# Kernel tuning notes

Hardware: AMD Instinct MI355X
Metric: run time of the kernel (lower is better)

Reference implementation:

```python
import jax, jax.numpy as jnp
import numpy as np

N_RET = 8192
N_LGN = 2048
SQUARE_SIZE = 10.0
NEIGHBOURHOOD = 1.0
MU_WTS = 2.5
SIGMA_WTS = 0.14
ETA = 0.1


def setup_inputs() -> dict:
    key = jax.random.key(0)
    ks = jax.random.split(key, 6)
    # retina topology on a [0, square_size]^2 plane
    topo = jax.random.uniform(ks[0], (N_RET, 2), dtype=jnp.float32) * SQUARE_SIZE
    # pairwise distances [N_ret, N_ret]
    d = jnp.sqrt(jnp.sum((topo[:, None, :] - topo[None, :, :]) ** 2, axis=-1))
    # per-node neighbourhood weights: normal(mu, sigma) masked to dist <= neighbourhood_size
    w = MU_WTS + SIGMA_WTS * jax.random.normal(ks[1], (N_RET, N_RET), dtype=jnp.float32)
    retina_weights = jnp.where(d <= NEIGHBOURHOOD, w, 0.0)
    # per-node firing threshold (Node internals: threshold ~ N(70, 2), same family as LGN)
    retina_threshold = 70.0 + 2.0 * jax.random.normal(ks[2], (N_RET,), dtype=jnp.float32)
    # LGN weights, row-normalised to mean mu_wts as in __init__
    lw = MU_WTS + SIGMA_WTS * jax.random.normal(ks[3], (N_LGN, N_RET), dtype=jnp.float32)
    lgn_weights = lw / jnp.mean(lw, axis=1, keepdims=True) * MU_WTS
    lgn_threshold = 70.0 + 2.0 * jax.random.normal(ks[4], (N_LGN,), dtype=jnp.float32)
    is_firing = (jax.random.uniform(ks[5], (N_RET,)) < 0.2).astype(jnp.float32)
    return {
        "retina_weights": retina_weights,
        "retina_threshold": retina_threshold,
        "lgn_weights": lgn_weights,
        "lgn_threshold": lgn_threshold,
        "is_firing": is_firing,
    }


def reference(retina_weights, retina_threshold, lgn_weights, lgn_threshold, is_firing):
    # Per-node sparse neighbourhood matvec (the Python loop over nodes, vectorised):
    node_x = retina_weights @ is_firing                       # [N_ret]
    new_firing = (node_x > retina_threshold).astype(retina_weights.dtype)
    # LGN activation + relu (lgn_act[lgn_act < 0] = 0)
    lgn_act = jnp.maximum(lgn_weights @ new_firing, 0.0)      # [N_lgn]
    act = jnp.maximum(lgn_act - lgn_threshold, 0.0)
    # winner-take-all update of the argmax LGN row
    idx = jnp.argmax(act)
    val = act[idx]
    row = lgn_weights[idx]
    # original does two additions of 0.5 * eta * val * active_neurons
    row = row + 0.5 * (ETA * val * new_firing)
    row = row + 0.5 * (ETA * val * new_firing)
    thr_new = lgn_threshold[idx] + 0.005 * val
    row = row / jnp.mean(row) * MU_WTS
    cond = val > 0
    lgn_weights_new = jnp.where(cond, lgn_weights.at[idx].set(row), lgn_weights)
    lgn_threshold_new = jnp.where(cond, lgn_threshold.at[idx].set(thr_new), lgn_threshold)
    return new_firing, lgn_act, lgn_weights_new, lgn_threshold_new
```

## Files before the change

kernel.cpp:

```cpp
#include <hip/hip_runtime.h>


constexpr int N_RET = 8192;
constexpr int N_LGN = 2048;
constexpr float ETA = 0.1f;
constexpr float MU_WTS = 2.5f;

typedef float vf4 __attribute__((ext_vector_type(4)));

__device__ __forceinline__ vf4 ntload4(const float* p) {
    return __builtin_nontemporal_load(reinterpret_cast<const vf4*>(p));
}
__device__ __forceinline__ void ntstore4(float* p, vf4 v) {
    __builtin_nontemporal_store(v, reinterpret_cast<vf4*>(p));
}
__device__ __forceinline__ vf4 ld4(const float* p) {
    return *reinterpret_cast<const vf4*>(p);
}
__device__ __forceinline__ void st4(float* p, vf4 v) {
    *reinterpret_cast<vf4*>(p) = v;
}

__global__ __launch_bounds__(256) void k_retina(
    const float* __restrict__ rw, const float* __restrict__ rthr,
    const float* __restrict__ firing, float* __restrict__ new_firing)
{
    const int t = threadIdx.x;
    const int lane = t & 63, wv = t >> 6;
    const int row = blockIdx.x * 4 + wv;
    const float* __restrict__ wr = rw + (size_t)row * N_RET;
    vf4 acc = (vf4)(0.0f);
#pragma unroll 8
    for (int it = 0; it < (N_RET / 4) / 64; ++it) {
        const int j = (lane + it * 64) * 4;
        acc += ntload4(wr + j) * ld4(firing + j);
    }
    float v = (acc.x + acc.y) + (acc.z + acc.w);
#pragma unroll
    for (int off = 32; off > 0; off >>= 1) v += __shfl_down(v, off, 64);
    if (lane == 0) new_firing[row] = (v > rthr[row]) ? 1.0f : 0.0f;
}

__global__ __launch_bounds__(256) void k_lgn(
    const float* __restrict__ lw, const float* __restrict__ firing,
    float* __restrict__ lgn_act, float* __restrict__ w_out)
{
    const int t = threadIdx.x;
    const int lane = t & 63, wv = t >> 6;
    const int row = blockIdx.x * 4 + wv;
    const float* __restrict__ wr = lw + (size_t)row * N_RET;
    float* __restrict__ wo = w_out + (size_t)row * N_RET;
    vf4 acc = (vf4)(0.0f);
#pragma unroll 8
    for (int it = 0; it < (N_RET / 4) / 64; ++it) {
        const int j = (lane + it * 64) * 4;
        const vf4 w = ntload4(wr + j);
        const vf4 f = ld4(firing + j);
        ntstore4(wo + j, w);
        acc += w * f;
    }
    float v = (acc.x + acc.y) + (acc.z + acc.w);
#pragma unroll
    for (int off = 32; off > 0; off >>= 1) v += __shfl_down(v, off, 64);
    if (lane == 0) lgn_act[row] = fmaxf(v, 0.0f);
}

__global__ __launch_bounds__(1024) void k_wta(
    const float* __restrict__ lgn_act, const float* __restrict__ lthr,
    const float* __restrict__ lw, const float* __restrict__ firing,
    float* __restrict__ thr_out, float* __restrict__ w_out)
{
    const int t = threadIdx.x;
    const int lane = t & 63, wv = t >> 6;
    __shared__ float sv[16];
    __shared__ int si[16];
    __shared__ float s_val, s_mean;
    __shared__ int s_idx;

    float bv = -1.0f;
    int bi = 0x40000000;
#pragma unroll
    for (int k = 0; k < N_LGN / 1024; ++k) {
        const int j = t + k * 1024;
        const float a = fmaxf(lgn_act[j] - lthr[j], 0.0f);
        if (a > bv) { bv = a; bi = j; }
    }
#pragma unroll
    for (int off = 32; off > 0; off >>= 1) {
        const float ov = __shfl_down(bv, off, 64);
        const int oi = __shfl_down(bi, off, 64);
        if (ov > bv || (ov == bv && oi < bi)) { bv = ov; bi = oi; }
    }
    if (lane == 0) { sv[wv] = bv; si[wv] = bi; }
    __syncthreads();
    if (t == 0) {
        float v = sv[0]; int i = si[0];
#pragma unroll
        for (int k = 1; k < 16; ++k)
            if (sv[k] > v || (sv[k] == v && si[k] < i)) { v = sv[k]; i = si[k]; }
        s_val = v; s_idx = i;
    }
    __syncthreads();
    const float val = s_val;
    const int idx = s_idx;

#pragma unroll
    for (int k = 0; k < N_LGN / 1024; ++k) {
        const int j = t + k * 1024;
        float tv = lthr[j];
        if (val > 0.0f && j == idx) tv += 0.005f * val;
        thr_out[j] = tv;
    }
    if (!(val > 0.0f)) return;

    const float* __restrict__ wr = lw + (size_t)idx * N_RET;
    float* __restrict__ wo = w_out + (size_t)idx * N_RET;
    const float av = 0.5f * (ETA * val);

    vf4 x[2];
    float part = 0.0f;
#pragma unroll
    for (int k = 0; k < (N_RET / 4) / 1024; ++k) {
        const int j = (t + k * 1024) * 4;
        const vf4 w = ld4(wr + j);
        const vf4 f = ld4(firing + j);
        vf4 v = (w + av * f) + av * f;
        x[k] = v;
        part += (v.x + v.y) + (v.z + v.w);
    }
#pragma unroll
    for (int off = 32; off > 0; off >>= 1) part += __shfl_down(part, off, 64);
    __shared__ float red[16];
    if (lane == 0) red[wv] = part;
    __syncthreads();
    if (t == 0) {
        float sum = 0.0f;
#pragma unroll
        for (int k = 0; k < 16; ++k) sum += red[k];
        s_mean = sum / (float)N_RET;
    }
    __syncthreads();
    const float m = s_mean;
#pragma unroll
    for (int k = 0; k < (N_RET / 4) / 1024; ++k) {
        const int j = (t + k * 1024) * 4;
        st4(wo + j, x[k] / m * MU_WTS);
    }
}

extern "C" void kernel_launch(void* const* d_in, const int* in_sizes, int n_in,
                              void* d_out, int out_size, void* d_ws, size_t ws_size,
                              hipStream_t stream)
{
    const float* rw   = (const float*)d_in[0];
    const float* rthr = (const float*)d_in[1];
    const float* lw   = (const float*)d_in[2];
    const float* lthr = (const float*)d_in[3];
    const float* fir  = (const float*)d_in[4];

    float* out   = (float*)d_out;
    float* o_fir = out;
    float* o_act = out + N_RET;
    float* o_w   = out + N_RET + N_LGN;
    float* o_thr = o_w + (size_t)N_LGN * N_RET;

    hipLaunchKernelGGL(k_retina, dim3(N_RET / 4), dim3(256),  0, stream, rw, rthr, fir, o_fir);
    hipLaunchKernelGGL(k_lgn,    dim3(N_LGN / 4), dim3(256),  0, stream, lw, o_fir, o_act, o_w);
    hipLaunchKernelGGL(k_wta,    dim3(1),         dim3(1024), 0, stream, o_act, lthr, lw, o_fir, o_thr, o_w);
}
```

Baseline: 75.12 us.

## Fuse WTA update into LGN kernel via last-block atomic counter

Merges the separate single-block winner-take-all kernel into the LGN matvec kernel. Each block increments a global counter after writing its activations, and the last block to finish does the argmax, threshold update and row renormalisation with 256 threads. This removes one kernel launch and its launch gap. In exchange the serial tail now runs on a smaller block, and correctness depends on the counter being reset by the retina kernel and on the atomic fences.

```diff
diff --git a/kernel.cpp b/kernel.cpp
--- a/kernel.cpp
+++ b/kernel.cpp
@@ -5,6 +5,7 @@
 constexpr int N_LGN = 2048;
 constexpr float ETA = 0.1f;
 constexpr float MU_WTS = 2.5f;
+constexpr int LGN_BLOCKS = N_LGN / 4;
 
 typedef float vf4 __attribute__((ext_vector_type(4)));
 
@@ -23,9 +24,11 @@
 
 __global__ __launch_bounds__(256) void k_retina(
     const float* __restrict__ rw, const float* __restrict__ rthr,
-    const float* __restrict__ firing, float* __restrict__ new_firing)
+    const float* __restrict__ firing, float* __restrict__ new_firing,
+    unsigned int* __restrict__ counter)
 {
     const int t = threadIdx.x;
+    if (blockIdx.x == 0 && t == 0) *counter = 0u;
     const int lane = t & 63, wv = t >> 6;
     const int row = blockIdx.x * 4 + wv;
     const float* __restrict__ wr = rw + (size_t)row * N_RET;
@@ -41,48 +44,59 @@
     if (lane == 0) new_firing[row] = (v > rthr[row]) ? 1.0f : 0.0f;
 }
 
-__global__ __launch_bounds__(256) void k_lgn(
+__global__ __launch_bounds__(256) void k_lgn_wta(
     const float* __restrict__ lw, const float* __restrict__ firing,
-    float* __restrict__ lgn_act, float* __restrict__ w_out)
+    const float* __restrict__ lthr,
+    float* __restrict__ lgn_act, float* __restrict__ w_out,
+    float* __restrict__ thr_out, unsigned int* __restrict__ counter)
 {
     const int t = threadIdx.x;
     const int lane = t & 63, wv = t >> 6;
-    const int row = blockIdx.x * 4 + wv;
-    const float* __restrict__ wr = lw + (size_t)row * N_RET;
-    float* __restrict__ wo = w_out + (size_t)row * N_RET;
-    vf4 acc = (vf4)(0.0f);
+
+    {
+        const int row = blockIdx.x * 4 + wv;
+        const float* __restrict__ wr = lw + (size_t)row * N_RET;
+        float* __restrict__ wo = w_out + (size_t)row * N_RET;
+        vf4 acc = (vf4)(0.0f);
 #pragma unroll 8
-    for (int it = 0; it < (N_RET / 4) / 64; ++it) {
-        const int j = (lane + it * 64) * 4;
-        const vf4 w = ntload4(wr + j);
-        const vf4 f = ld4(firing + j);
-        ntstore4(wo + j, w);
-        acc += w * f;
+        for (int it = 0; it < (N_RET / 4) / 64; ++it) {
+            const int j = (lane + it * 64) * 4;
+            const vf4 w = ntload4(wr + j);
+            const vf4 f = ld4(firing + j);
+            ntstore4(wo + j, w);
+            acc += w * f;
+        }
+        float v = (acc.x + acc.y) + (acc.z + acc.w);
+#pragma unroll
+        for (int off = 32; off > 0; off >>= 1) v += __shfl_down(v, off, 64);
+        if (lane == 0) lgn_act[row] = fmaxf(v, 0.0f);
     }
-    float v = (acc.x + acc.y) + (acc.z + acc.w);
-#pragma unroll
-    for (int off = 32; off > 0; off >>= 1) v += __shfl_down(v, off, 64);
-    if (lane == 0) lgn_act[row] = fmaxf(v, 0.0f);
-}
 
-__global__ __launch_bounds__(1024) void k_wta(
-    const float* __restrict__ lgn_act, const float* __restrict__ lthr,
-    const float* __restrict__ lw, const float* __restrict__ firing,
-    float* __restrict__ thr_out, float* __restrict__ w_out)
-{
-    const int t = threadIdx.x;
-    const int lane = t & 63, wv = t >> 6;
-    __shared__ float sv[16];
-    __shared__ int si[16];
+    __shared__ bool s_last;
+    __syncthreads();
+    if (t == 0) {
+        __threadfence();
+        const unsigned old = __hip_atomic_fetch_add(counter, 1u,
+                                                    __ATOMIC_ACQ_REL,
+                                                    __HIP_MEMORY_SCOPE_AGENT);
+        s_last = (old == (unsigned)(gridDim.x - 1));
+    }
+    __syncthreads();
+    if (!s_last) return;
+
+    __shared__ float sv[4];
+    __shared__ int si[4];
     __shared__ float s_val, s_mean;
     __shared__ int s_idx;
 
     float bv = -1.0f;
     int bi = 0x40000000;
 #pragma unroll
-    for (int k = 0; k < N_LGN / 1024; ++k) {
-        const int j = t + k * 1024;
-        const float a = fmaxf(lgn_act[j] - lthr[j], 0.0f);
+    for (int k = 0; k < N_LGN / 256; ++k) {
+        const int j = t + k * 256;
+        const float aj = __hip_atomic_load(&lgn_act[j], __ATOMIC_ACQUIRE,
+                                           __HIP_MEMORY_SCOPE_AGENT);
+        const float a = fmaxf(aj - lthr[j], 0.0f);
         if (a > bv) { bv = a; bi = j; }
     }
 #pragma unroll
@@ -96,7 +110,7 @@
     if (t == 0) {
         float v = sv[0]; int i = si[0];
 #pragma unroll
-        for (int k = 1; k < 16; ++k)
+        for (int k = 1; k < 4; ++k)
             if (sv[k] > v || (sv[k] == v && si[k] < i)) { v = sv[k]; i = si[k]; }
         s_val = v; s_idx = i;
     }
@@ -105,8 +119,8 @@
     const int idx = s_idx;
 
 #pragma unroll
-    for (int k = 0; k < N_LGN / 1024; ++k) {
-        const int j = t + k * 1024;
+    for (int k = 0; k < N_LGN / 256; ++k) {
+        const int j = t + k * 256;
         float tv = lthr[j];
         if (val > 0.0f && j == idx) tv += 0.005f * val;
         thr_out[j] = tv;
@@ -117,11 +131,11 @@
     float* __restrict__ wo = w_out + (size_t)idx * N_RET;
     const float av = 0.5f * (ETA * val);
 
-    vf4 x[2];
+    vf4 x[(N_RET / 4) / 256];
     float part = 0.0f;
 #pragma unroll
-    for (int k = 0; k < (N_RET / 4) / 1024; ++k) {
-        const int j = (t + k * 1024) * 4;
+    for (int k = 0; k < (N_RET / 4) / 256; ++k) {
+        const int j = (t + k * 256) * 4;
         const vf4 w = ld4(wr + j);
         const vf4 f = ld4(firing + j);
         vf4 v = (w + av * f) + av * f;
@@ -130,20 +144,14 @@
     }
 #pragma unroll
     for (int off = 32; off > 0; off >>= 1) part += __shfl_down(part, off, 64);
-    __shared__ float red[16];
-    if (lane == 0) red[wv] = part;
+    if (lane == 0) sv[wv] = part;
     __syncthreads();
-    if (t == 0) {
-        float sum = 0.0f;
-#pragma unroll
-        for (int k = 0; k < 16; ++k) sum += red[k];
-        s_mean = sum / (float)N_RET;
-    }
+    if (t == 0) s_mean = ((sv[0] + sv[1]) + (sv[2] + sv[3])) / (float)N_RET;
     __syncthreads();
     const float m = s_mean;
 #pragma unroll
-    for (int k = 0; k < (N_RET / 4) / 1024; ++k) {
-        const int j = (t + k * 1024) * 4;
+    for (int k = 0; k < (N_RET / 4) / 256; ++k) {
+        const int j = (t + k * 256) * 4;
         st4(wo + j, x[k] / m * MU_WTS);
     }
 }
@@ -163,8 +171,10 @@
     float* o_act = out + N_RET;
     float* o_w   = out + N_RET + N_LGN;
     float* o_thr = o_w + (size_t)N_LGN * N_RET;
+    unsigned int* counter = (unsigned int*)d_ws;
 
-    hipLaunchKernelGGL(k_retina, dim3(N_RET / 4), dim3(256),  0, stream, rw, rthr, fir, o_fir);
-    hipLaunchKernelGGL(k_lgn,    dim3(N_LGN / 4), dim3(256),  0, stream, lw, o_fir, o_act, o_w);
-    hipLaunchKernelGGL(k_wta,    dim3(1),         dim3(1024), 0, stream, o_act, lthr, lw, o_fir, o_thr, o_w);
+    hipLaunchKernelGGL(k_retina,  dim3(N_RET / 4), dim3(256), 0, stream,
+                       rw, rthr, fir, o_fir, counter);
+    hipLaunchKernelGGL(k_lgn_wta, dim3(LGN_BLOCKS), dim3(256), 0, stream,
+                       lw, o_fir, lthr, o_act, o_w, o_thr, counter);
 }
```

After: 122.0 us. +62.4%, slower.
